# Optimization experiments

Measured on AMD Instinct MI355X. Metric: run time of the kernel, lower is better.

## Reference

```python
import jax, jax.numpy as jnp
import numpy as np

NUM_LAYERS = 32
NUM_SLOTS = 128
HIDDEN = 4096
T_WRITE = 128   # == NUM_SLOTS so slot_ids form a permutation (deterministic scatter)
T_READ = 8192
EMA_ALPHA = 0.1


def setup_inputs() -> dict:
    key = jax.random.key(0)
    ks = jax.random.split(key, 4)
    values = jax.random.normal(ks[0], (T_WRITE, HIDDEN), jnp.float32)
    queries = jax.random.normal(ks[1], (T_READ, HIDDEN), jnp.float32)
    memory = jax.random.normal(ks[2], (NUM_LAYERS, NUM_SLOTS, HIDDEN), jnp.float32) * 0.02
    gate_w = jax.random.normal(ks[3], (NUM_LAYERS, HIDDEN), jnp.float32) * (1.0 / np.sqrt(HIDDEN))
    gate_b = jnp.zeros((NUM_LAYERS,), jnp.float32)
    return {
        "values": values,
        "queries": queries,
        "memory": memory,
        "gate_w": gate_w,
        "gate_b": gate_b,
        "layer_idx": 0,
        "k": 8,
        "ptr": 0,
    }


def reference(values, queries, memory, gate_w, gate_b, layer_idx, k, ptr):
    # ---- write(): EMA scatter into one layer's slots ----
    mem_l = memory[layer_idx]                                  # [N, d]
    g = jax.nn.sigmoid(values @ gate_w[layer_idx] + gate_b[layer_idx])[:, None]  # [T,1]
    T = values.shape[0]
    slot_ids = (ptr + jnp.arange(T)) % NUM_SLOTS               # [T]
    current = mem_l[slot_ids]                                  # gather [T, d]
    updated = EMA_ALPHA * g * values + (1.0 - EMA_ALPHA) * current
    mem_new = mem_l.at[slot_ids].set(updated)                  # scatter-write [N, d]

    # ---- read(): matmul -> top-k -> gather -> softmax -> weighted sum ----
    scale = 1.0 / jnp.sqrt(jnp.float32(HIDDEN))
    scores = (queries @ mem_new.T) * scale                     # [T_read, N]
    topk_scores, topk_idx = jax.lax.top_k(scores, k)           # [T_read, k]
    attn = jax.nn.softmax(topk_scores, axis=-1)                # [T_read, k]
    topk_v = mem_new[topk_idx]                                 # gather [T_read, k, d]
    out = jnp.einsum('tk,tkd->td', attn, topk_v)               # [T_read, d]
    return out
```

## Files before the change

### kernel.cpp

```cpp
#include <hip/hip_runtime.h>
#include <math.h>

#define D 4096
#define NSLOTS 128
#define TR 8192
#define NKQ 8
#define KCH 512
#define EPS_TRIG 1e-3f
#define WIN 5e-4f

typedef __attribute__((ext_vector_type(8))) short bf16x8;
typedef __attribute__((ext_vector_type(4))) float f32x4;

union BV { bf16x8 v; unsigned u[4]; };

__device__ __forceinline__ unsigned short bfrne(float x) {
  unsigned u = __float_as_uint(x);
  unsigned r = u + 0x7fffu + ((u >> 16) & 1u);
  return (unsigned short)(r >> 16);
}

__device__ __forceinline__ void gload16(const void* gsrc, void* ldst) {
  __builtin_amdgcn_global_load_lds(
      (const __attribute__((address_space(1))) void*)gsrc,
      (__attribute__((address_space(3))) void*)ldst, 16, 0, 0);
}

__global__ __launch_bounds__(256) void update_mem_kernel(
    const float* __restrict__ values, const float* __restrict__ memory,
    const float* __restrict__ gate_w, const float* __restrict__ gate_b,
    const int* __restrict__ layer_idx_p, const int* __restrict__ ptr_p,
    int T_W, float* __restrict__ ws_mem,
    unsigned short* __restrict__ MFh,
    unsigned short* __restrict__ BTFh, unsigned short* __restrict__ BTFm) {
  const int l = layer_idx_p[0], p = ptr_p[0], s = blockIdx.x, tid = threadIdx.x;
  int t0 = ((s - p) % NSLOTS + NSLOTS) % NSLOTS;
  const bool written = (t0 < T_W);
  const int t = written ? (t0 + ((T_W - 1 - t0) / NSLOTS) * NSLOTS) : 0;
  const float* mrow = memory + ((size_t)l * NSLOTS + s) * D;
  const float* vrow = values + (size_t)t * D;

  float acoef = 0.f, bcoef = 1.0f;
  if (written) {
    const float* gw = gate_w + (size_t)l * D;
    double acc = 0.0;
    for (int j = tid; j < D; j += 256)
      acc += (double)vrow[j] * (double)gw[j];
    for (int off = 32; off; off >>= 1) acc += __shfl_down(acc, off, 64);
    __shared__ double wsum[4];
    if ((tid & 63) == 0) wsum[tid >> 6] = acc;
    __syncthreads();
    double dot = wsum[0] + wsum[1] + wsum[2] + wsum[3];
    float x = (float)dot + gate_b[l];
    float g = 1.0f / (1.0f + expf(-x));
    acoef = 0.1f * g; bcoef = 0.9f;
  }

  const int sg = s >> 4, fr_s = s & 15;
  const int ksS = s >> 5, foS = (s >> 3) & 3, posS = s & 7;
  for (int j8 = tid; j8 < D / 8; j8 += 256) {
    float4 mv0 = ((const float4*)mrow)[j8 * 2];
    float4 mv1 = ((const float4*)mrow)[j8 * 2 + 1];
    float4 vv0 = make_float4(0.f, 0.f, 0.f, 0.f), vv1 = vv0;
    if (written) {
      vv0 = ((const float4*)vrow)[j8 * 2];
      vv1 = ((const float4*)vrow)[j8 * 2 + 1];
    }
    float ov[8];
    ov[0] = acoef * vv0.x + bcoef * mv0.x;
    ov[1] = acoef * vv0.y + bcoef * mv0.y;
    ov[2] = acoef * vv0.z + bcoef * mv0.z;
    ov[3] = acoef * vv0.w + bcoef * mv0.w;
    ov[4] = acoef * vv1.x + bcoef * mv1.x;
    ov[5] = acoef * vv1.y + bcoef * mv1.y;
    ov[6] = acoef * vv1.z + bcoef * mv1.z;
    ov[7] = acoef * vv1.w + bcoef * mv1.w;
    ((float4*)(ws_mem + (size_t)s * D))[j8 * 2] =
        make_float4(ov[0], ov[1], ov[2], ov[3]);
    ((float4*)(ws_mem + (size_t)s * D))[j8 * 2 + 1] =
        make_float4(ov[4], ov[5], ov[6], ov[7]);

    unsigned short h[8], md[8];
#pragma unroll
    for (int e = 0; e < 8; ++e) {
      h[e] = bfrne(ov[e]);
      float f = __uint_as_float((unsigned)h[e] << 16);
      md[e] = bfrne(ov[e] - f);
    }
    const int ks = j8 >> 2, fo = j8 & 3;
    const size_t unit = (size_t)ks * 512 + sg * 64 + fo * 16 + fr_s;
    uint4 hp;
    hp.x = (unsigned)h[0] | ((unsigned)h[1] << 16);
    hp.y = (unsigned)h[2] | ((unsigned)h[3] << 16);
    hp.z = (unsigned)h[4] | ((unsigned)h[5] << 16);
    hp.w = (unsigned)h[6] | ((unsigned)h[7] << 16);
    ((uint4*)MFh)[unit] = hp;
#pragma unroll
    for (int e = 0; e < 8; ++e) {
      int c = j8 * 8 + e;
      size_t u = ((size_t)(c >> 4) * 4 + ksS) * 64 + foS * 16 + (c & 15);
      BTFh[u * 8 + posS] = h[e];
      BTFm[u * 8 + posS] = md[e];
    }
  }
}

__global__ __launch_bounds__(256) void scores_kernel(
    const float* __restrict__ queries, const unsigned short* __restrict__ MFh,
    float* __restrict__ part) {
  __shared__ float Qs[4][4096];

  const int tid = threadIdx.x, lane = tid & 63, w = tid >> 6;
  const int fr = lane & 15, fo = lane >> 4;
  const int qt = blockIdx.x >> 3, kq = blockIdx.x & (NKQ - 1);
  const int qbase = qt * 128;
  const int kbase = kq * KCH;

  const int rl = lane >> 3, ul = lane & 7;
  const int su = ul ^ rl;
  const float* qsrc[4];
#pragma unroll
  for (int i = 0; i < 4; ++i) {
    int dl = w * 4 + i;
    qsrc[i] = queries + (size_t)(qbase + 8 * dl + rl) * D + kbase + su * 4;
  }
  const unsigned short* bsrc = MFh + (size_t)kq * 16 * 4096 + (size_t)lane * 8;

  f32x4 acc[2][8];
#pragma unroll
  for (int rg = 0; rg < 2; ++rg)
#pragma unroll
    for (int cg = 0; cg < 8; ++cg) acc[rg][cg] = (f32x4){0.f, 0.f, 0.f, 0.f};

  const int rowA = w * 32 + fr;

#define STGQ(B_, S_) do {                                                    \
    _Pragma("unroll")                                                        \
    for (int i = 0; i < 4; ++i)                                              \
      gload16(qsrc[i] + (S_) * 32, &Qs[B_][(w * 4 + i) * 256]);              \
  } while (0)

  STGQ(0, 0);
  STGQ(1, 1);
#pragma unroll
  for (int s = 0; s < 16; ++s) {
    bf16x8 bh_[8];
#pragma unroll
    for (int cg = 0; cg < 8; ++cg)
      bh_[cg] = *(const bf16x8*)(bsrc + (size_t)s * 4096 + cg * 64 * 8);
    if (s + 2 < 16) STGQ((s + 2) & 3, s + 2);
    if (s <= 13) asm volatile("s_waitcnt vmcnt(4)" ::: "memory");
    else         asm volatile("s_waitcnt vmcnt(0)" ::: "memory");
    __builtin_amdgcn_sched_barrier(0);
    __builtin_amdgcn_s_barrier();
#pragma unroll
    for (int rg = 0; rg < 2; ++rg) {
      const int row = rowA + rg * 16;
      float4 a0 = *(const float4*)&Qs[s & 3][row * 32 + (((fo * 2) ^ (row & 7)) << 2)];
      float4 a1 = *(const float4*)&Qs[s & 3][row * 32 + ((((fo * 2) | 1) ^ (row & 7)) << 2)];
      float qf[8] = {a0.x, a0.y, a0.z, a0.w, a1.x, a1.y, a1.z, a1.w};
      BV ah;
#pragma unroll
      for (int i = 0; i < 4; ++i) {
        unsigned u0 = __float_as_uint(qf[2 * i]);
        unsigned u1 = __float_as_uint(qf[2 * i + 1]);
        ah.u[i] = (u0 >> 16) | (u1 & 0xffff0000u);
      }
#pragma unroll
      for (int cg = 0; cg < 8; ++cg)
        acc[rg][cg] = __builtin_amdgcn_mfma_f32_16x16x32_bf16(ah.v, bh_[cg], acc[rg][cg], 0, 0, 0);
    }
  }
#undef STGQ

  float* op = part + ((size_t)kq * TR + qbase) * NSLOTS;
#pragma unroll
  for (int rg = 0; rg < 2; ++rg)
#pragma unroll
    for (int cg = 0; cg < 8; ++cg)
#pragma unroll
      for (int r = 0; r < 4; ++r)
        op[(size_t)(w * 32 + rg * 16 + fo * 4 + r) * NSLOTS + cg * 16 + fr] =
            acc[rg][cg][r];
}

__device__ __forceinline__ unsigned mapf(float f) {
  unsigned u = __float_as_uint(f);
  return (u & 0x80000000u) ? ~u : (u | 0x80000000u);
}
__device__ __forceinline__ float unmapf(unsigned u) {
  return __uint_as_float((u & 0x80000000u) ? (u & 0x7fffffffu) : ~u);
}

__device__ __forceinline__ void wave_select(
    float va, float vb, int l, int k, int iters,
    float &m, float &sum, bool &sela, bool &selb, float &vkm1, float &vkk) {
  m = 0.f; sum = 0.f; sela = false; selb = false; vkm1 = 0.f; vkk = -3.4e38f;
  for (int it = 0; it < iters; ++it) {
    unsigned long long ka =
        ((unsigned long long)mapf(va) << 32) | (unsigned)(127 - l);
    unsigned long long kb =
        ((unsigned long long)mapf(vb) << 32) | (unsigned)(63 - l);
    unsigned long long key = ka > kb ? ka : kb;
#pragma unroll
    for (int off = 32; off; off >>= 1) {
      unsigned long long o = __shfl_xor(key, off, 64);
      if (o > key) key = o;
    }
    int idx = 127 - (int)(unsigned)(key & 0xffffffffULL);
    float val = unmapf((unsigned)(key >> 32));
    if (it == 0) m = val;
    if (it < k) sum += expf(val - m);
    if (it == k - 1) vkm1 = val;
    if (it == k) vkk = val;
    if (idx == l) { sela = sela || (it < k); va = -INFINITY; }
    if (idx == l + 64) { selb = selb || (it < k); vb = -INFINITY; }
  }
}

__device__ __forceinline__ float rescore_slot(const float* __restrict__ qrow,
                                              const float* __restrict__ mrow,
                                              int l) {
  double acc = 0.0;
#pragma unroll 4
  for (int c = 0; c < 16; ++c) {
    int j = c * 256 + l * 4;
    float4 qv = *(const float4*)(qrow + j);
    float4 mv = *(const float4*)(mrow + j);
    acc += (double)qv.x * (double)mv.x;
    acc += (double)qv.y * (double)mv.y;
    acc += (double)qv.z * (double)mv.z;
    acc += (double)qv.w * (double)mv.w;
  }
#pragma unroll
  for (int off = 32; off; off >>= 1) acc += __shfl_xor(acc, off, 64);
  return (float)(acc * 0.015625);
}

__global__ __launch_bounds__(256) void topk_kernel(
    const float* __restrict__ part, const float* __restrict__ ws_mem,
    const float* __restrict__ queries, const int* __restrict__ k_p,
    unsigned short* __restrict__ AFh, unsigned short* __restrict__ AFm) {
  const int w = threadIdx.x >> 6, l = threadIdx.x & 63;
  const int row = blockIdx.x * 4 + w;
  int k = k_p[0];
  if (k < 1) k = 1;
  if (k > NSLOTS) k = NSLOTS;
  const int ksel = (k < NSLOTS) ? k + 1 : k;

  float origa = 0.f, origb = 0.f;
#pragma unroll
  for (int kq = 0; kq < NKQ; ++kq) {
    origa += part[((size_t)kq * TR + row) * NSLOTS + l];
    origb += part[((size_t)kq * TR + row) * NSLOTS + 64 + l];
  }
  origa *= 0.015625f;
  origb *= 0.015625f;

  float m, sum, vkm1, vkk;
  bool sela, selb;
  wave_select(origa, origb, l, k, ksel, m, sum, sela, selb, vkm1, vkk);

  if (ksel > k && (vkm1 - vkk) < EPS_TRIG) {
    const float* qrow = queries + (size_t)row * D;
    float lo = vkk - WIN, hi = vkm1 + WIN;
    unsigned long long ba = __ballot(origa >= lo && origa <= hi);
    unsigned long long bb = __ballot(origb >= lo && origb <= hi);
    while (ba) {
      int s = __ffsll(ba) - 1; ba &= ba - 1;
      float ex = rescore_slot(qrow, ws_mem + (size_t)s * D, l);
      if (l == s) origa = ex;
    }
    while (bb) {
      int s = __ffsll(bb) - 1; bb &= bb - 1;
      float ex = rescore_slot(qrow, ws_mem + (size_t)(s + 64) * D, l);
      if (l == s) origb = ex;
    }
    wave_select(origa, origb, l, k, k, m, sum, sela, selb, vkm1, vkk);
  }

  const float inv = 1.0f / sum;
  float wa = sela ? expf(origa - m) * inv : 0.f;
  float wb = selb ? expf(origb - m) * inv : 0.f;

  unsigned short ha = bfrne(wa);
  unsigned short ma = bfrne(wa - __uint_as_float((unsigned)ha << 16));
  unsigned short hb = bfrne(wb);
  unsigned short mb = bfrne(wb - __uint_as_float((unsigned)hb << 16));

  const int rg = row >> 4, frr = row & 15;
  const size_t ua =
      (((size_t)rg * 4 + (l >> 5)) * 64 + ((l >> 3) & 3) * 16 + frr) * 8 + (l & 7);
  const size_t ub =
      (((size_t)rg * 4 + (l >> 5) + 2) * 64 + ((l >> 3) & 3) * 16 + frr) * 8 + (l & 7);
  AFh[ua] = ha; AFm[ua] = ma;
  AFh[ub] = hb; AFm[ub] = mb;
}

__global__ __launch_bounds__(256) void gather_kernel(
    const unsigned short* __restrict__ AFh, const unsigned short* __restrict__ AFm,
    const unsigned short* __restrict__ BTFh, const unsigned short* __restrict__ BTFm,
    float* __restrict__ out) {
  const int tid = threadIdx.x, lane = tid & 63, w = tid >> 6;
  const int fr = lane & 15, fo = lane >> 4;
  const int rowblk = blockIdx.x >> 5, colblk = blockIdx.x & 31;
  const int r0 = rowblk * 128 + w * 32;
  const int rg0 = r0 >> 4;

  bf16x8 a_h[2][4], a_m[2][4];
#pragma unroll
  for (int rg = 0; rg < 2; ++rg)
#pragma unroll
    for (int ks = 0; ks < 4; ++ks) {
      const size_t u = (((size_t)(rg0 + rg) * 4 + ks) * 64 + lane) * 8;
      a_h[rg][ks] = *(const bf16x8*)(AFh + u);
      a_m[rg][ks] = *(const bf16x8*)(AFm + u);
    }

#pragma unroll 2
  for (int cgi = 0; cgi < 8; ++cgi) {
    const int cg = colblk * 8 + cgi;
    bf16x8 b_h[4], b_m[4];
#pragma unroll
    for (int ks = 0; ks < 4; ++ks) {
      const size_t u = (((size_t)cg * 4 + ks) * 64 + lane) * 8;
      b_h[ks] = *(const bf16x8*)(BTFh + u);
      b_m[ks] = *(const bf16x8*)(BTFm + u);
    }
    const int col = cg * 16 + fr;
#pragma unroll
    for (int rg = 0; rg < 2; ++rg) {
      f32x4 acc = {0.f, 0.f, 0.f, 0.f};
#pragma unroll
      for (int ks = 0; ks < 4; ++ks) {
        acc = __builtin_amdgcn_mfma_f32_16x16x32_bf16(a_m[rg][ks], b_h[ks], acc, 0, 0, 0);
        acc = __builtin_amdgcn_mfma_f32_16x16x32_bf16(a_h[rg][ks], b_m[ks], acc, 0, 0, 0);
        acc = __builtin_amdgcn_mfma_f32_16x16x32_bf16(a_h[rg][ks], b_h[ks], acc, 0, 0, 0);
      }
#pragma unroll
      for (int r = 0; r < 4; ++r)
        out[(size_t)(r0 + rg * 16 + fo * 4 + r) * D + col] = acc[r];
    }
  }
}

extern "C" void kernel_launch(void* const* d_in, const int* in_sizes, int n_in,
                              void* d_out, int out_size, void* d_ws, size_t ws_size,
                              hipStream_t stream) {
  const float* values  = (const float*)d_in[0];
  const float* queries = (const float*)d_in[1];
  const float* memory  = (const float*)d_in[2];
  const float* gate_w  = (const float*)d_in[3];
  const float* gate_b  = (const float*)d_in[4];
  const int* layer_idx = (const int*)d_in[5];
  const int* k_p       = (const int*)d_in[6];
  const int* ptr_p     = (const int*)d_in[7];

  const int T_W = in_sizes[0] / D;
  const int T_R = in_sizes[1] / D;

  float* ws_mem = (float*)d_ws;
  float* part   = ws_mem + (size_t)NSLOTS * D;
  unsigned short* MFh  = (unsigned short*)(part + (size_t)NKQ * TR * NSLOTS);
  unsigned short* BTFh = MFh  + (size_t)NSLOTS * D;
  unsigned short* BTFm = BTFh + (size_t)NSLOTS * D;
  unsigned short* AFh  = BTFm + (size_t)NSLOTS * D;
  unsigned short* AFm  = AFh  + (size_t)T_R * NSLOTS;

  update_mem_kernel<<<NSLOTS, 256, 0, stream>>>(
      values, memory, gate_w, gate_b, layer_idx, ptr_p, T_W,
      ws_mem, MFh, BTFh, BTFm);
  scores_kernel<<<(T_R / 128) * NKQ, 256, 0, stream>>>(queries, MFh, part);
  topk_kernel<<<T_R / 4, 256, 0, stream>>>(part, ws_mem, queries, k_p, AFh, AFm);
  gather_kernel<<<(T_R / 128) * (D / 128), 256, 0, stream>>>(AFh, AFm, BTFh, BTFm,
                                                             (float*)d_out);
}
```

Before: 133.1 us.

## Load query tiles directly into registers and halve rows per block in scores kernel

The scores kernel stops staging queries through LDS with async global-to-LDS copies and barriers. Each lane now loads its own query fragment straight into registers with a 4-deep prefetch ring, and the B fragments are double-buffered across k-steps. The tile shrinks from 128 to 64 query rows per block, so the grid doubles and each B fragment load is reused by half as many rows. This removes LDS traffic and block barriers in exchange for more global loads of B and less reuse per block.

Result: slower. 147.7 us (+11.0%).

```diff
diff --git a/kernel.cpp b/kernel.cpp
--- a/kernel.cpp
+++ b/kernel.cpp
@@ -18,12 +18,6 @@
   unsigned u = __float_as_uint(x);
   unsigned r = u + 0x7fffu + ((u >> 16) & 1u);
   return (unsigned short)(r >> 16);
-}
-
-__device__ __forceinline__ void gload16(const void* gsrc, void* ldst) {
-  __builtin_amdgcn_global_load_lds(
-      (const __attribute__((address_space(1))) void*)gsrc,
-      (__attribute__((address_space(3))) void*)ldst, 16, 0, 0);
 }
 
 __global__ __launch_bounds__(256) void update_mem_kernel(
@@ -108,80 +102,64 @@
 __global__ __launch_bounds__(256) void scores_kernel(
     const float* __restrict__ queries, const unsigned short* __restrict__ MFh,
     float* __restrict__ part) {
-  __shared__ float Qs[4][4096];
-
   const int tid = threadIdx.x, lane = tid & 63, w = tid >> 6;
   const int fr = lane & 15, fo = lane >> 4;
   const int qt = blockIdx.x >> 3, kq = blockIdx.x & (NKQ - 1);
-  const int qbase = qt * 128;
+  const int qbase = qt * 64;
   const int kbase = kq * KCH;
 
-  const int rl = lane >> 3, ul = lane & 7;
-  const int su = ul ^ rl;
-  const float* qsrc[4];
-#pragma unroll
-  for (int i = 0; i < 4; ++i) {
-    int dl = w * 4 + i;
-    qsrc[i] = queries + (size_t)(qbase + 8 * dl + rl) * D + kbase + su * 4;
-  }
+  const float* qp = queries + (size_t)(qbase + w * 16 + fr) * D + kbase + fo * 8;
   const unsigned short* bsrc = MFh + (size_t)kq * 16 * 4096 + (size_t)lane * 8;
 
-  f32x4 acc[2][8];
-#pragma unroll
-  for (int rg = 0; rg < 2; ++rg)
-#pragma unroll
-    for (int cg = 0; cg < 8; ++cg) acc[rg][cg] = (f32x4){0.f, 0.f, 0.f, 0.f};
-
-  const int rowA = w * 32 + fr;
-
-#define STGQ(B_, S_) do {                                                    \
-    _Pragma("unroll")                                                        \
-    for (int i = 0; i < 4; ++i)                                              \
-      gload16(qsrc[i] + (S_) * 32, &Qs[B_][(w * 4 + i) * 256]);              \
-  } while (0)
-
-  STGQ(0, 0);
-  STGQ(1, 1);
+  f32x4 acc[8];
+#pragma unroll
+  for (int cg = 0; cg < 8; ++cg) acc[cg] = (f32x4){0.f, 0.f, 0.f, 0.f};
+
+  float4 qA[4][2];
+  bf16x8 qB[2][8];
+
+#pragma unroll
+  for (int i = 0; i < 2; ++i) {
+    qA[i][0] = *(const float4*)(qp + i * 32);
+    qA[i][1] = *(const float4*)(qp + i * 32 + 4);
+  }
+#pragma unroll
+  for (int cg = 0; cg < 8; ++cg)
+    qB[0][cg] = *(const bf16x8*)(bsrc + cg * 512);
+
 #pragma unroll
   for (int s = 0; s < 16; ++s) {
-    bf16x8 bh_[8];
+    if (s + 2 < 16) {
+      qA[(s + 2) & 3][0] = *(const float4*)(qp + (s + 2) * 32);
+      qA[(s + 2) & 3][1] = *(const float4*)(qp + (s + 2) * 32 + 4);
+    }
+    if (s + 1 < 16) {
+#pragma unroll
+      for (int cg = 0; cg < 8; ++cg)
+        qB[(s + 1) & 1][cg] =
+            *(const bf16x8*)(bsrc + (size_t)(s + 1) * 4096 + cg * 512);
+    }
+    float4 a0 = qA[s & 3][0], a1 = qA[s & 3][1];
+    float qf[8] = {a0.x, a0.y, a0.z, a0.w, a1.x, a1.y, a1.z, a1.w};
+    BV ah;
+#pragma unroll
+    for (int i = 0; i < 4; ++i) {
+      unsigned u0 = __float_as_uint(qf[2 * i]);
+      unsigned u1 = __float_as_uint(qf[2 * i + 1]);
+      ah.u[i] = (u0 >> 16) | (u1 & 0xffff0000u);
+    }
 #pragma unroll
     for (int cg = 0; cg < 8; ++cg)
-      bh_[cg] = *(const bf16x8*)(bsrc + (size_t)s * 4096 + cg * 64 * 8);
-    if (s + 2 < 16) STGQ((s + 2) & 3, s + 2);
-    if (s <= 13) asm volatile("s_waitcnt vmcnt(4)" ::: "memory");
-    else         asm volatile("s_waitcnt vmcnt(0)" ::: "memory");
-    __builtin_amdgcn_sched_barrier(0);
-    __builtin_amdgcn_s_barrier();
-#pragma unroll
-    for (int rg = 0; rg < 2; ++rg) {
-      const int row = rowA + rg * 16;
-      float4 a0 = *(const float4*)&Qs[s & 3][row * 32 + (((fo * 2) ^ (row & 7)) << 2)];
-      float4 a1 = *(const float4*)&Qs[s & 3][row * 32 + ((((fo * 2) | 1) ^ (row & 7)) << 2)];
-      float qf[8] = {a0.x, a0.y, a0.z, a0.w, a1.x, a1.y, a1.z, a1.w};
-      BV ah;
-#pragma unroll
-      for (int i = 0; i < 4; ++i) {
-        unsigned u0 = __float_as_uint(qf[2 * i]);
-        unsigned u1 = __float_as_uint(qf[2 * i + 1]);
-        ah.u[i] = (u0 >> 16) | (u1 & 0xffff0000u);
-      }
-#pragma unroll
-      for (int cg = 0; cg < 8; ++cg)
-        acc[rg][cg] = __builtin_amdgcn_mfma_f32_16x16x32_bf16(ah.v, bh_[cg], acc[rg][cg], 0, 0, 0);
-    }
-  }
-#undef STGQ
+      acc[cg] = __builtin_amdgcn_mfma_f32_16x16x32_bf16(ah.v, qB[s & 1][cg],
+                                                        acc[cg], 0, 0, 0);
+  }
 
   float* op = part + ((size_t)kq * TR + qbase) * NSLOTS;
 #pragma unroll
-  for (int rg = 0; rg < 2; ++rg)
-#pragma unroll
-    for (int cg = 0; cg < 8; ++cg)
-#pragma unroll
-      for (int r = 0; r < 4; ++r)
-        op[(size_t)(w * 32 + rg * 16 + fo * 4 + r) * NSLOTS + cg * 16 + fr] =
-            acc[rg][cg][r];
+  for (int cg = 0; cg < 8; ++cg)
+#pragma unroll
+    for (int r = 0; r < 4; ++r)
+      op[(size_t)(w * 16 + fo * 4 + r) * NSLOTS + cg * 16 + fr] = acc[cg][r];
 }
 
 __device__ __forceinline__ unsigned mapf(float f) {
@@ -370,7 +348,7 @@
   update_mem_kernel<<<NSLOTS, 256, 0, stream>>>(
       values, memory, gate_w, gate_b, layer_idx, ptr_p, T_W,
       ws_mem, MFh, BTFh, BTFm);
-  scores_kernel<<<(T_R / 128) * NKQ, 256, 0, stream>>>(queries, MFh, part);
+  scores_kernel<<<(T_R / 64) * NKQ, 256, 0, stream>>>(queries, MFh, part);
   topk_kernel<<<T_R / 4, 256, 0, stream>>>(part, ws_mem, queries, k_p, AFh, AFm);
   gather_kernel<<<(T_R / 128) * (D / 128), 256, 0, stream>>>(AFh, AFm, BTFh, BTFm,
                                                              (float*)d_out);
```
